# Performance work log

Hardware: AMD Instinct MI355X
Metric: run time of the kernel (lower is better)

## Reference

```python
import jax, jax.numpy as jnp
import numpy as np

D_MODEL = 1024
NUM_HEADS = 16
D_K = D_MODEL // NUM_HEADS


def setup_inputs() -> dict:
    key = jax.random.key(0)
    k1, k2, k3, k4 = jax.random.split(key, 4)
    x = jax.random.normal(k1, (2, 2048, D_MODEL), dtype=jnp.float32)
    # qkv_proj: Linear(d_model, 3*d_model, bias=False); stored as [in, out] for x @ W
    W_qkv = jax.random.normal(k2, (D_MODEL, 3 * D_MODEL), dtype=jnp.float32) * (1.0 / np.sqrt(D_MODEL))
    W_out = jax.random.normal(k3, (D_MODEL, D_MODEL), dtype=jnp.float32) * (1.0 / np.sqrt(D_MODEL))
    b_out = jax.random.normal(k4, (D_MODEL,), dtype=jnp.float32) * 0.01
    return {"x": x, "W_qkv": W_qkv, "W_out": W_out, "b_out": b_out}


def reference(x, W_qkv, W_out, b_out):
    B, N, C = x.shape
    scale = 1.0 / np.sqrt(D_K)
    qkv = (x @ W_qkv).reshape(B, N, 3, NUM_HEADS, D_K)
    qkv = jnp.transpose(qkv, (2, 0, 3, 1, 4))  # [3, B, H, N, d_k]
    q, k, v = qkv[0], qkv[1], qkv[2]
    scores = jnp.einsum("bhqd,bhkd->bhqk", q, k) * scale  # [B,H,N,N]
    attn = jax.nn.softmax(scores, axis=-1)
    out = jnp.einsum("bhqk,bhkd->bhqd", attn, v)  # [B,H,N,d_k]
    out = jnp.transpose(out, (0, 2, 1, 3)).reshape(B, N, C)
    return out @ W_out + b_out
```

## Files before the change

kernel.cpp:

```cpp
#include <hip/hip_runtime.h>
#include <cstdint>

typedef __bf16 bf16_t;
typedef __bf16 bf16x8 __attribute__((ext_vector_type(8)));
typedef float  f32x4  __attribute__((ext_vector_type(4)));
typedef uint32_t u32x4 __attribute__((ext_vector_type(4)));

#define MFMA16(a,b,c) __builtin_amdgcn_mfma_f32_16x16x32_bf16((a),(b),(c),0,0,0)

__device__ __forceinline__ void gload_lds16(const bf16_t* g, bf16_t* l) {
  __builtin_amdgcn_global_load_lds(
      (const __attribute__((address_space(1))) unsigned int*)g,
      (__attribute__((address_space(3))) unsigned int*)l,
      16, 0, 0);
}

__device__ __forceinline__ uint32_t cvt_pk_bf16(float lo, float hi) {
  uint32_t r;
  asm("v_cvt_pk_bf16_f32 %0, %1, %2" : "=v"(r) : "v"(lo), "v"(hi));
  return r;
}

__global__ void k_conv_x(const float* __restrict__ x, bf16_t* __restrict__ xb) {
  int i = blockIdx.x * blockDim.x + threadIdx.x;
  const float4* p = reinterpret_cast<const float4*>(x) + (size_t)i * 2;
  float4 a = p[0], b = p[1];
  bf16x8 v;
  v[0]=(bf16_t)a.x; v[1]=(bf16_t)a.y; v[2]=(bf16_t)a.z; v[3]=(bf16_t)a.w;
  v[4]=(bf16_t)b.x; v[5]=(bf16_t)b.y; v[6]=(bf16_t)b.z; v[7]=(bf16_t)b.w;
  *reinterpret_cast<bf16x8*>(xb + (size_t)i * 8) = v;
}

__global__ void k_transpose_w(const float* __restrict__ W, bf16_t* __restrict__ WT,
                              int K, int N) {
  __shared__ float tile[32][33];
  int n0 = blockIdx.x * 32, k0 = blockIdx.y * 32;
  int c = threadIdx.x & 31, r8 = threadIdx.x >> 5;
#pragma unroll
  for (int rr = 0; rr < 4; rr++) {
    int r = r8 + rr * 8;
    tile[r][c] = W[(size_t)(k0 + r) * N + n0 + c];
  }
  __syncthreads();
#pragma unroll
  for (int rr = 0; rr < 4; rr++) {
    int r = r8 + rr * 8;
    WT[(size_t)(n0 + r) * K + k0 + c] = (bf16_t)tile[c][r];
  }
}

__global__ void k_vtrans(const bf16_t* __restrict__ V, bf16_t* __restrict__ VT) {
  __shared__ bf16_t t[64 * 72];
  int bi = blockIdx.x;
  int head = bi >> 5, kt = bi & 31;
  int tid = threadIdx.x;
  const bf16_t* src = V + (size_t)head * 131072 + (size_t)kt * 64 * 64;
#pragma unroll
  for (int j = 0; j < 2; j++) {
    int q = tid + 256 * j;
    int key = q >> 3, part = q & 7;
    bf16x8 v = *reinterpret_cast<const bf16x8*>(src + key * 64 + part * 8);
    *reinterpret_cast<bf16x8*>(&t[key * 72 + part * 8]) = v;
  }
  __syncthreads();
  bf16_t* dst = VT + (size_t)head * 131072 + kt * 64;
#pragma unroll
  for (int j = 0; j < 2; j++) {
    int q = tid + 256 * j;
    int dv = q >> 3, part = q & 7;
    bf16x8 v;
#pragma unroll
    for (int e = 0; e < 8; e++) v[e] = t[(part * 8 + e) * 72 + dv];
    *reinterpret_cast<bf16x8*>(dst + (size_t)dv * 2048 + part * 8) = v;
  }
}

template<int EPI>
__global__ __launch_bounds__(256, 2) void k_gemm(
    const bf16_t* __restrict__ A, const bf16_t* __restrict__ BT, int Klen,
    bf16_t* __restrict__ Qo, bf16_t* __restrict__ Ko, bf16_t* __restrict__ Vo,
    const float* __restrict__ bias, float* __restrict__ Out, int Nout) {
  __shared__ bf16_t As[2][4096];
  __shared__ bf16_t Bs[2][4096];
  int tid = threadIdx.x, lane = tid & 63, wid = tid >> 6;
  int row0 = blockIdx.x * 128, col0 = blockIdx.y * 128;
  int wr = wid >> 1, wc = wid & 1;
  int g = lane >> 4, li = lane & 15;

  f32x4 acc[4][4] = {};

  auto stage = [&](int buf, int kt) {
    int k0 = kt * 32;
#pragma unroll
    for (int j = 0; j < 2; j++) {
      int q = tid + 256 * j;
      int r = q >> 2, part = q & 3;
      gload_lds16(A + (size_t)(row0 + r) * Klen + k0 + part * 8,
                  &As[buf][(wid * 64 + j * 256) * 8]);
    }
#pragma unroll
    for (int j = 0; j < 2; j++) {
      int q = tid + 256 * j;
      int r = q >> 2, part = q & 3;
      gload_lds16(BT + (size_t)(col0 + r) * Klen + k0 + part * 8,
                  &Bs[buf][(wid * 64 + j * 256) * 8]);
    }
  };

  int nk = Klen >> 5;
  stage(0, 0);
  for (int kt = 0; kt < nk; kt++) {
    __syncthreads();
    if (kt + 1 < nk) stage((kt + 1) & 1, kt + 1);
    int buf = kt & 1;
    int kl = g * 8;
    bf16x8 a[4], b[4];
#pragma unroll
    for (int m = 0; m < 4; m++)
      a[m] = *reinterpret_cast<const bf16x8*>(&As[buf][(wr * 64 + m * 16 + li) * 32 + kl]);
#pragma unroll
    for (int n = 0; n < 4; n++)
      b[n] = *reinterpret_cast<const bf16x8*>(&Bs[buf][(wc * 64 + n * 16 + li) * 32 + kl]);
#pragma unroll
    for (int m = 0; m < 4; m++)
#pragma unroll
      for (int n = 0; n < 4; n++)
        acc[m][n] = MFMA16(a[m], b[n], acc[m][n]);
  }

#pragma unroll
  for (int m = 0; m < 4; m++) {
    int rg = row0 + wr * 64 + m * 16 + g * 4;
#pragma unroll
    for (int n = 0; n < 4; n++) {
      int cg = col0 + wc * 64 + n * 16 + li;
#pragma unroll
      for (int i = 0; i < 4; i++) {
        float v = acc[m][n][i];
        int row = rg + i;
        if constexpr (EPI == 0) {
          int t = cg >> 10, h = (cg >> 6) & 15, dk = cg & 63;
          int b2 = row >> 11, nn = row & 2047;
          size_t idx = ((size_t)((b2 << 4) + h) * 2048 + nn) * 64 + dk;
          if (t == 0)      Qo[idx] = (bf16_t)(v * 0.18033688011112042f);
          else if (t == 1) Ko[idx] = (bf16_t)v;
          else             Vo[idx] = (bf16_t)v;
        } else {
          Out[(size_t)row * Nout + cg] = v + bias[cg];
        }
      }
    }
  }
}

__global__ __launch_bounds__(256, 4) void k_flash(
    const bf16_t* __restrict__ Q, const bf16_t* __restrict__ K,
    const bf16_t* __restrict__ VT, bf16_t* __restrict__ O) {
  __shared__ bf16_t Ks[2][64 * 64];
  __shared__ bf16_t Vs[2][64 * 64];

  int bi = (blockIdx.x & 7) * 128 + (blockIdx.x >> 3);
  int head = bi >> 5, qt = bi & 31;
  int tid = threadIdx.x, lane = tid & 63, wid = tid >> 6;
  int g = lane >> 4, li = lane & 15;

  const bf16_t* Qh = Q + (size_t)head * 131072 + (size_t)qt * 64 * 64;
  const bf16_t* Kh = K + (size_t)head * 131072;
  const bf16_t* Vh = VT + (size_t)head * 131072;

  bf16x8 qf[2];
  {
    const bf16_t* qrow = Qh + (size_t)(wid * 16 + li) * 64;
    qf[0] = *reinterpret_cast<const bf16x8*>(qrow + g * 8);
    qf[1] = *reinterpret_cast<const bf16x8*>(qrow + 32 + g * 8);
  }

  u32x4 onesw;
  onesw[0] = 0x3F803F80u; onesw[1] = 0x3F803F80u;
  onesw[2] = 0x3F803F80u; onesw[3] = 0x3F803F80u;
  bf16x8 ones = __builtin_bit_cast(bf16x8, onesw);

  f32x4 o[4] = {};
  f32x4 osum = {};
  float mrun = 0.f;

  auto stage = [&](int buf, int t) {
    int kv0 = t * 64;
#pragma unroll
    for (int j = 0; j < 2; j++) {
      int q = tid + 256 * j;
      int key = q >> 3, part = q & 7;
      int sw = (key & 7) ^ (((key >> 3) & 3) << 1);
      gload_lds16(Kh + (size_t)(kv0 + key) * 64 + ((part ^ sw) * 8),
                  &Ks[buf][(wid * 64 + j * 256) * 8]);
    }
#pragma unroll
    for (int j = 0; j < 2; j++) {
      int q = tid + 256 * j;
      int dv = q >> 3, part = q & 7;
      gload_lds16(Vh + (size_t)dv * 2048 + kv0 + ((part ^ (dv & 7)) * 8),
                  &Vs[buf][(wid * 64 + j * 256) * 8]);
    }
  };

  stage(0, 0);
  for (int t = 0; t < 32; t++) {
    __syncthreads();
    if (t + 1 < 32) stage((t + 1) & 1, t + 1);
    int buf = t & 1;
    char* KsB = (char*)&Ks[buf][0];
    char* VsB = (char*)&Vs[buf][0];

    float nm = -mrun;
    f32x4 s[4];
#pragma unroll
    for (int nf = 0; nf < 4; nf++) { s[nf][0]=nm; s[nf][1]=nm; s[nf][2]=nm; s[nf][3]=nm; }
    __builtin_amdgcn_s_setprio(1);
#pragma unroll
    for (int kd = 0; kd < 2; kd++)
#pragma unroll
      for (int nf = 0; nf < 4; nf++) {
        int key = ((li >> 2) << 3) | ((nf & 1) << 2) | (li & 3) | ((nf >> 1) << 5);
        int sw = (key & 7) ^ (((key >> 3) & 3) << 1);
        bf16x8 a = *reinterpret_cast<const bf16x8*>(
            KsB + key * 128 + (((kd * 4 + g) ^ sw) << 4));
        s[nf] = MFMA16(a, qf[kd], s[nf]);
      }
    __builtin_amdgcn_s_setprio(0);

    float t0 = fmaxf(fmaxf(s[0][0], s[0][1]), s[0][2]);
    float t1 = fmaxf(fmaxf(s[0][3], s[1][0]), s[1][1]);
    float t2 = fmaxf(fmaxf(s[1][2], s[1][3]), s[2][0]);
    float t3 = fmaxf(fmaxf(s[2][1], s[2][2]), s[2][3]);
    float t4 = fmaxf(fmaxf(s[3][0], s[3][1]), s[3][2]);
    float pmax = fmaxf(fmaxf(fmaxf(t0, t1), fmaxf(t2, t3)), fmaxf(t4, s[3][3]));

    if (!__all(pmax <= 8.f)) {
      float v = pmax;
      v = fmaxf(v, __shfl_xor(v, 16));
      v = fmaxf(v, __shfl_xor(v, 32));
      float d = fmaxf(v, 0.f);
      float sc = __builtin_amdgcn_exp2f(-d);
      mrun += d;
#pragma unroll
      for (int nf = 0; nf < 4; nf++)
#pragma unroll
        for (int i = 0; i < 4; i++) s[nf][i] -= d;
      float osc[4];
#pragma unroll
      for (int i = 0; i < 4; i++) osc[i] = __shfl(sc, g * 4 + i);
#pragma unroll
      for (int nf = 0; nf < 4; nf++)
#pragma unroll
        for (int i = 0; i < 4; i++) o[nf][i] *= osc[i];
#pragma unroll
      for (int i = 0; i < 4; i++) osum[i] *= osc[i];
    }

#pragma unroll
    for (int nf = 0; nf < 4; nf++)
#pragma unroll
      for (int i = 0; i < 4; i++)
        s[nf][i] = __builtin_amdgcn_exp2f(s[nf][i]);

    u32x4 w0, w1;
    w0[0] = cvt_pk_bf16(s[0][0], s[0][1]);
    w0[1] = cvt_pk_bf16(s[0][2], s[0][3]);
    w0[2] = cvt_pk_bf16(s[1][0], s[1][1]);
    w0[3] = cvt_pk_bf16(s[1][2], s[1][3]);
    w1[0] = cvt_pk_bf16(s[2][0], s[2][1]);
    w1[1] = cvt_pk_bf16(s[2][2], s[2][3]);
    w1[2] = cvt_pk_bf16(s[3][0], s[3][1]);
    w1[3] = cvt_pk_bf16(s[3][2], s[3][3]);
    bf16x8 pa0 = __builtin_bit_cast(bf16x8, w0);
    bf16x8 pa1 = __builtin_bit_cast(bf16x8, w1);

    __builtin_amdgcn_s_setprio(1);
    osum = MFMA16(pa0, ones, osum);
    osum = MFMA16(pa1, ones, osum);
#pragma unroll
    for (int nfv = 0; nfv < 4; nfv++) {
      int dv = nfv * 16 + li;
      bf16x8 b0 = *reinterpret_cast<const bf16x8*>(
          VsB + dv * 128 + ((g * 16) ^ ((dv & 7) << 4)));
      o[nfv] = MFMA16(pa0, b0, o[nfv]);
      bf16x8 b1 = *reinterpret_cast<const bf16x8*>(
          VsB + dv * 128 + ((64 + g * 16) ^ ((dv & 7) << 4)));
      o[nfv] = MFMA16(pa1, b1, o[nfv]);
    }
    __builtin_amdgcn_s_setprio(0);
  }

  int b2 = head >> 4, h = head & 15;
#pragma unroll
  for (int i = 0; i < 4; i++) {
    float inv = 1.f / osum[i];
    int n = qt * 64 + wid * 16 + g * 4 + i;
    size_t base = ((size_t)b2 * 2048 + n) * 1024 + h * 64;
#pragma unroll
    for (int nfv = 0; nfv < 4; nfv++)
      O[base + nfv * 16 + li] = (bf16_t)(o[nfv][i] * inv);
  }
}

extern "C" void kernel_launch(void* const* d_in, const int* in_sizes, int n_in,
                              void* d_out, int out_size, void* d_ws, size_t ws_size,
                              hipStream_t stream) {
  const float* x    = (const float*)d_in[0];
  const float* Wqkv = (const float*)d_in[1];
  const float* Wout = (const float*)d_in[2];
  const float* bout = (const float*)d_in[3];
  float* out = (float*)d_out;

  char* ws = (char*)d_ws;
  bf16_t* xb    = (bf16_t*)(ws);
  bf16_t* wqkvT = (bf16_t*)(ws + ((size_t)8  << 20));
  bf16_t* woutT = (bf16_t*)(ws + ((size_t)14 << 20));
  bf16_t* qw    = (bf16_t*)(ws + ((size_t)16 << 20));
  bf16_t* kw    = (bf16_t*)(ws + ((size_t)24 << 20));
  bf16_t* vw    = (bf16_t*)(ws + ((size_t)32 << 20));
  bf16_t* vtw   = (bf16_t*)(ws + ((size_t)40 << 20));
  bf16_t* ow    = (bf16_t*)(ws + ((size_t)48 << 20));

  k_conv_x<<<2048, 256, 0, stream>>>(x, xb);
  k_transpose_w<<<dim3(96, 32), 256, 0, stream>>>(Wqkv, wqkvT, 1024, 3072);
  k_transpose_w<<<dim3(32, 32), 256, 0, stream>>>(Wout, woutT, 1024, 1024);
  k_gemm<0><<<dim3(32, 24), 256, 0, stream>>>(xb, wqkvT, 1024, qw, kw, vw,
                                              nullptr, nullptr, 0);
  k_vtrans<<<1024, 256, 0, stream>>>(vw, vtw);
  k_flash<<<1024, 256, 0, stream>>>(qw, kw, vtw, ow);
  k_gemm<1><<<dim3(32, 8), 256, 0, stream>>>(ow, woutT, 1024,
                                             nullptr, nullptr, nullptr,
                                             bout, out, 1024);
}
```

Before: 125.2 us.

## Double query rows per flash block and use 64-row tiles for output GEMM

The flash kernel now processes 128 query rows per block, two 16-row groups per wave. Each K and V fragment read from LDS is reused across both groups, which halves K/V staging traffic per query and the block count. The output GEMM is templated to use 64-row tiles, doubling its grid to 512 blocks so more CUs are busy. The trade-offs are higher register pressure in flash (launch bounds relaxed from 4 to 2), fewer flash blocks (512) for latency hiding, and more B-tile reloads in the output GEMM.

```diff
diff --git a/kernel.cpp b/kernel.cpp
--- a/kernel.cpp
+++ b/kernel.cpp
@@ -75,35 +75,37 @@
   }
 }
 
-template<int EPI>
+template<int EPI, int MT>
 __global__ __launch_bounds__(256, 2) void k_gemm(
     const bf16_t* __restrict__ A, const bf16_t* __restrict__ BT, int Klen,
     bf16_t* __restrict__ Qo, bf16_t* __restrict__ Ko, bf16_t* __restrict__ Vo,
     const float* __restrict__ bias, float* __restrict__ Out, int Nout) {
-  __shared__ bf16_t As[2][4096];
+  constexpr int WM = MT / 2;
+  constexpr int MF = WM / 16;
+  __shared__ bf16_t As[2][MT * 32];
   __shared__ bf16_t Bs[2][4096];
   int tid = threadIdx.x, lane = tid & 63, wid = tid >> 6;
-  int row0 = blockIdx.x * 128, col0 = blockIdx.y * 128;
+  int row0 = blockIdx.x * MT, col0 = blockIdx.y * 128;
   int wr = wid >> 1, wc = wid & 1;
   int g = lane >> 4, li = lane & 15;
 
-  f32x4 acc[4][4] = {};
+  f32x4 acc[MF][4] = {};
 
   auto stage = [&](int buf, int kt) {
     int k0 = kt * 32;
 #pragma unroll
-    for (int j = 0; j < 2; j++) {
+    for (int j = 0; j < MT / 64; j++) {
       int q = tid + 256 * j;
       int r = q >> 2, part = q & 3;
       gload_lds16(A + (size_t)(row0 + r) * Klen + k0 + part * 8,
-                  &As[buf][(wid * 64 + j * 256) * 8]);
+                  &As[buf][q * 8]);
     }
 #pragma unroll
     for (int j = 0; j < 2; j++) {
       int q = tid + 256 * j;
       int r = q >> 2, part = q & 3;
       gload_lds16(BT + (size_t)(col0 + r) * Klen + k0 + part * 8,
-                  &Bs[buf][(wid * 64 + j * 256) * 8]);
+                  &Bs[buf][q * 8]);
     }
   };
 
@@ -114,23 +116,23 @@
     if (kt + 1 < nk) stage((kt + 1) & 1, kt + 1);
     int buf = kt & 1;
     int kl = g * 8;
-    bf16x8 a[4], b[4];
-#pragma unroll
-    for (int m = 0; m < 4; m++)
-      a[m] = *reinterpret_cast<const bf16x8*>(&As[buf][(wr * 64 + m * 16 + li) * 32 + kl]);
+    bf16x8 a[MF], b[4];
+#pragma unroll
+    for (int m = 0; m < MF; m++)
+      a[m] = *reinterpret_cast<const bf16x8*>(&As[buf][(wr * WM + m * 16 + li) * 32 + kl]);
 #pragma unroll
     for (int n = 0; n < 4; n++)
       b[n] = *reinterpret_cast<const bf16x8*>(&Bs[buf][(wc * 64 + n * 16 + li) * 32 + kl]);
 #pragma unroll
-    for (int m = 0; m < 4; m++)
+    for (int m = 0; m < MF; m++)
 #pragma unroll
       for (int n = 0; n < 4; n++)
         acc[m][n] = MFMA16(a[m], b[n], acc[m][n]);
   }
 
 #pragma unroll
-  for (int m = 0; m < 4; m++) {
-    int rg = row0 + wr * 64 + m * 16 + g * 4;
+  for (int m = 0; m < MF; m++) {
+    int rg = row0 + wr * WM + m * 16 + g * 4;
 #pragma unroll
     for (int n = 0; n < 4; n++) {
       int cg = col0 + wc * 64 + n * 16 + li;
@@ -153,26 +155,27 @@
   }
 }
 
-__global__ __launch_bounds__(256, 4) void k_flash(
+__global__ __launch_bounds__(256, 2) void k_flash(
     const bf16_t* __restrict__ Q, const bf16_t* __restrict__ K,
     const bf16_t* __restrict__ VT, bf16_t* __restrict__ O) {
   __shared__ bf16_t Ks[2][64 * 64];
   __shared__ bf16_t Vs[2][64 * 64];
 
-  int bi = (blockIdx.x & 7) * 128 + (blockIdx.x >> 3);
-  int head = bi >> 5, qt = bi & 31;
+  int bi = (blockIdx.x & 7) * 64 + (blockIdx.x >> 3);
+  int head = bi >> 4, qt = bi & 15;
   int tid = threadIdx.x, lane = tid & 63, wid = tid >> 6;
   int g = lane >> 4, li = lane & 15;
 
-  const bf16_t* Qh = Q + (size_t)head * 131072 + (size_t)qt * 64 * 64;
+  const bf16_t* Qh = Q + (size_t)head * 131072 + (size_t)qt * 128 * 64;
   const bf16_t* Kh = K + (size_t)head * 131072;
   const bf16_t* Vh = VT + (size_t)head * 131072;
 
-  bf16x8 qf[2];
-  {
-    const bf16_t* qrow = Qh + (size_t)(wid * 16 + li) * 64;
-    qf[0] = *reinterpret_cast<const bf16x8*>(qrow + g * 8);
-    qf[1] = *reinterpret_cast<const bf16x8*>(qrow + 32 + g * 8);
+  bf16x8 qf[2][2];
+#pragma unroll
+  for (int rg = 0; rg < 2; rg++) {
+    const bf16_t* qrow = Qh + (size_t)(wid * 32 + rg * 16 + li) * 64;
+    qf[rg][0] = *reinterpret_cast<const bf16x8*>(qrow + g * 8);
+    qf[rg][1] = *reinterpret_cast<const bf16x8*>(qrow + 32 + g * 8);
   }
 
   u32x4 onesw;
@@ -180,9 +183,9 @@
   onesw[2] = 0x3F803F80u; onesw[3] = 0x3F803F80u;
   bf16x8 ones = __builtin_bit_cast(bf16x8, onesw);
 
-  f32x4 o[4] = {};
-  f32x4 osum = {};
-  float mrun = 0.f;
+  f32x4 o[2][4] = {};
+  f32x4 osum[2] = {};
+  float mrun[2] = {0.f, 0.f};
 
   auto stage = [&](int buf, int t) {
     int kv0 = t * 64;
@@ -192,14 +195,14 @@
       int key = q >> 3, part = q & 7;
       int sw = (key & 7) ^ (((key >> 3) & 3) << 1);
       gload_lds16(Kh + (size_t)(kv0 + key) * 64 + ((part ^ sw) * 8),
-                  &Ks[buf][(wid * 64 + j * 256) * 8]);
+                  &Ks[buf][(tid + j * 256) * 8]);
     }
 #pragma unroll
     for (int j = 0; j < 2; j++) {
       int q = tid + 256 * j;
       int dv = q >> 3, part = q & 7;
       gload_lds16(Vh + (size_t)dv * 2048 + kv0 + ((part ^ (dv & 7)) * 8),
-                  &Vs[buf][(wid * 64 + j * 256) * 8]);
+                  &Vs[buf][(tid + j * 256) * 8]);
     }
   };
 
@@ -211,95 +214,126 @@
     char* KsB = (char*)&Ks[buf][0];
     char* VsB = (char*)&Vs[buf][0];
 
-    float nm = -mrun;
-    f32x4 s[4];
-#pragma unroll
-    for (int nf = 0; nf < 4; nf++) { s[nf][0]=nm; s[nf][1]=nm; s[nf][2]=nm; s[nf][3]=nm; }
-    __builtin_amdgcn_s_setprio(1);
+    bf16x8 ka[2][4];
 #pragma unroll
     for (int kd = 0; kd < 2; kd++)
 #pragma unroll
       for (int nf = 0; nf < 4; nf++) {
         int key = ((li >> 2) << 3) | ((nf & 1) << 2) | (li & 3) | ((nf >> 1) << 5);
         int sw = (key & 7) ^ (((key >> 3) & 3) << 1);
-        bf16x8 a = *reinterpret_cast<const bf16x8*>(
+        ka[kd][nf] = *reinterpret_cast<const bf16x8*>(
             KsB + key * 128 + (((kd * 4 + g) ^ sw) << 4));
-        s[nf] = MFMA16(a, qf[kd], s[nf]);
+      }
+
+    f32x4 s[2][4];
+#pragma unroll
+    for (int rg = 0; rg < 2; rg++) {
+      float nm = -mrun[rg];
+#pragma unroll
+      for (int nf = 0; nf < 4; nf++) {
+        s[rg][nf][0] = nm; s[rg][nf][1] = nm; s[rg][nf][2] = nm; s[rg][nf][3] = nm;
+      }
+    }
+    __builtin_amdgcn_s_setprio(1);
+#pragma unroll
+    for (int kd = 0; kd < 2; kd++)
+#pragma unroll
+      for (int nf = 0; nf < 4; nf++) {
+        s[0][nf] = MFMA16(ka[kd][nf], qf[0][kd], s[0][nf]);
+        s[1][nf] = MFMA16(ka[kd][nf], qf[1][kd], s[1][nf]);
       }
     __builtin_amdgcn_s_setprio(0);
 
-    float t0 = fmaxf(fmaxf(s[0][0], s[0][1]), s[0][2]);
-    float t1 = fmaxf(fmaxf(s[0][3], s[1][0]), s[1][1]);
-    float t2 = fmaxf(fmaxf(s[1][2], s[1][3]), s[2][0]);
-    float t3 = fmaxf(fmaxf(s[2][1], s[2][2]), s[2][3]);
-    float t4 = fmaxf(fmaxf(s[3][0], s[3][1]), s[3][2]);
-    float pmax = fmaxf(fmaxf(fmaxf(t0, t1), fmaxf(t2, t3)), fmaxf(t4, s[3][3]));
-
-    if (!__all(pmax <= 8.f)) {
-      float v = pmax;
-      v = fmaxf(v, __shfl_xor(v, 16));
-      v = fmaxf(v, __shfl_xor(v, 32));
-      float d = fmaxf(v, 0.f);
-      float sc = __builtin_amdgcn_exp2f(-d);
-      mrun += d;
+    float pmax[2];
+#pragma unroll
+    for (int rg = 0; rg < 2; rg++) {
+      float t0 = fmaxf(fmaxf(s[rg][0][0], s[rg][0][1]), s[rg][0][2]);
+      float t1 = fmaxf(fmaxf(s[rg][0][3], s[rg][1][0]), s[rg][1][1]);
+      float t2 = fmaxf(fmaxf(s[rg][1][2], s[rg][1][3]), s[rg][2][0]);
+      float t3 = fmaxf(fmaxf(s[rg][2][1], s[rg][2][2]), s[rg][2][3]);
+      float t4 = fmaxf(fmaxf(s[rg][3][0], s[rg][3][1]), s[rg][3][2]);
+      pmax[rg] = fmaxf(fmaxf(fmaxf(t0, t1), fmaxf(t2, t3)), fmaxf(t4, s[rg][3][3]));
+    }
+
+    bool ok = (pmax[0] <= 8.f) & (pmax[1] <= 8.f);
+    if (!__all(ok)) {
+#pragma unroll
+      for (int rg = 0; rg < 2; rg++) {
+        float v = pmax[rg];
+        v = fmaxf(v, __shfl_xor(v, 16));
+        v = fmaxf(v, __shfl_xor(v, 32));
+        float d = fmaxf(v, 0.f);
+        float sc = __builtin_amdgcn_exp2f(-d);
+        mrun[rg] += d;
+#pragma unroll
+        for (int nf = 0; nf < 4; nf++)
+#pragma unroll
+          for (int i = 0; i < 4; i++) s[rg][nf][i] -= d;
+        float osc[4];
+#pragma unroll
+        for (int i = 0; i < 4; i++) osc[i] = __shfl(sc, g * 4 + i);
+#pragma unroll
+        for (int nf = 0; nf < 4; nf++)
+#pragma unroll
+          for (int i = 0; i < 4; i++) o[rg][nf][i] *= osc[i];
+#pragma unroll
+        for (int i = 0; i < 4; i++) osum[rg][i] *= osc[i];
+      }
+    }
+
+    bf16x8 pa[2][2];
+#pragma unroll
+    for (int rg = 0; rg < 2; rg++) {
 #pragma unroll
       for (int nf = 0; nf < 4; nf++)
 #pragma unroll
-        for (int i = 0; i < 4; i++) s[nf][i] -= d;
-      float osc[4];
-#pragma unroll
-      for (int i = 0; i < 4; i++) osc[i] = __shfl(sc, g * 4 + i);
-#pragma unroll
-      for (int nf = 0; nf < 4; nf++)
-#pragma unroll
-        for (int i = 0; i < 4; i++) o[nf][i] *= osc[i];
-#pragma unroll
-      for (int i = 0; i < 4; i++) osum[i] *= osc[i];
-    }
-
-#pragma unroll
-    for (int nf = 0; nf < 4; nf++)
-#pragma unroll
-      for (int i = 0; i < 4; i++)
-        s[nf][i] = __builtin_amdgcn_exp2f(s[nf][i]);
-
-    u32x4 w0, w1;
-    w0[0] = cvt_pk_bf16(s[0][0], s[0][1]);
-    w0[1] = cvt_pk_bf16(s[0][2], s[0][3]);
-    w0[2] = cvt_pk_bf16(s[1][0], s[1][1]);
-    w0[3] = cvt_pk_bf16(s[1][2], s[1][3]);
-    w1[0] = cvt_pk_bf16(s[2][0], s[2][1]);
-    w1[1] = cvt_pk_bf16(s[2][2], s[2][3]);
-    w1[2] = cvt_pk_bf16(s[3][0], s[3][1]);
-    w1[3] = cvt_pk_bf16(s[3][2], s[3][3]);
-    bf16x8 pa0 = __builtin_bit_cast(bf16x8, w0);
-    bf16x8 pa1 = __builtin_bit_cast(bf16x8, w1);
+        for (int i = 0; i < 4; i++)
+          s[rg][nf][i] = __builtin_amdgcn_exp2f(s[rg][nf][i]);
+      u32x4 w0, w1;
+      w0[0] = cvt_pk_bf16(s[rg][0][0], s[rg][0][1]);
+      w0[1] = cvt_pk_bf16(s[rg][0][2], s[rg][0][3]);
+      w0[2] = cvt_pk_bf16(s[rg][1][0], s[rg][1][1]);
+      w0[3] = cvt_pk_bf16(s[rg][1][2], s[rg][1][3]);
+      w1[0] = cvt_pk_bf16(s[rg][2][0], s[rg][2][1]);
+      w1[1] = cvt_pk_bf16(s[rg][2][2], s[rg][2][3]);
+      w1[2] = cvt_pk_bf16(s[rg][3][0], s[rg][3][1]);
+      w1[3] = cvt_pk_bf16(s[rg][3][2], s[rg][3][3]);
+      pa[rg][0] = __builtin_bit_cast(bf16x8, w0);
+      pa[rg][1] = __builtin_bit_cast(bf16x8, w1);
+    }
 
     __builtin_amdgcn_s_setprio(1);
-    osum = MFMA16(pa0, ones, osum);
-    osum = MFMA16(pa1, ones, osum);
+    osum[0] = MFMA16(pa[0][0], ones, osum[0]);
+    osum[0] = MFMA16(pa[0][1], ones, osum[0]);
+    osum[1] = MFMA16(pa[1][0], ones, osum[1]);
+    osum[1] = MFMA16(pa[1][1], ones, osum[1]);
 #pragma unroll
     for (int nfv = 0; nfv < 4; nfv++) {
       int dv = nfv * 16 + li;
       bf16x8 b0 = *reinterpret_cast<const bf16x8*>(
           VsB + dv * 128 + ((g * 16) ^ ((dv & 7) << 4)));
-      o[nfv] = MFMA16(pa0, b0, o[nfv]);
       bf16x8 b1 = *reinterpret_cast<const bf16x8*>(
           VsB + dv * 128 + ((64 + g * 16) ^ ((dv & 7) << 4)));
-      o[nfv] = MFMA16(pa1, b1, o[nfv]);
+      o[0][nfv] = MFMA16(pa[0][0], b0, o[0][nfv]);
+      o[0][nfv] = MFMA16(pa[0][1], b1, o[0][nfv]);
+      o[1][nfv] = MFMA16(pa[1][0], b0, o[1][nfv]);
+      o[1][nfv] = MFMA16(pa[1][1], b1, o[1][nfv]);
     }
     __builtin_amdgcn_s_setprio(0);
   }
 
   int b2 = head >> 4, h = head & 15;
 #pragma unroll
-  for (int i = 0; i < 4; i++) {
-    float inv = 1.f / osum[i];
-    int n = qt * 64 + wid * 16 + g * 4 + i;
-    size_t base = ((size_t)b2 * 2048 + n) * 1024 + h * 64;
-#pragma unroll
-    for (int nfv = 0; nfv < 4; nfv++)
-      O[base + nfv * 16 + li] = (bf16_t)(o[nfv][i] * inv);
+  for (int rg = 0; rg < 2; rg++) {
+#pragma unroll
+    for (int i = 0; i < 4; i++) {
+      float inv = 1.f / osum[rg][i];
+      int n = qt * 128 + wid * 32 + rg * 16 + g * 4 + i;
+      size_t base = ((size_t)b2 * 2048 + n) * 1024 + h * 64;
+#pragma unroll
+      for (int nfv = 0; nfv < 4; nfv++)
+        O[base + nfv * 16 + li] = (bf16_t)(o[rg][nfv][i] * inv);
+    }
   }
 }
 
@@ -325,11 +359,11 @@
   k_conv_x<<<2048, 256, 0, stream>>>(x, xb);
   k_transpose_w<<<dim3(96, 32), 256, 0, stream>>>(Wqkv, wqkvT, 1024, 3072);
   k_transpose_w<<<dim3(32, 32), 256, 0, stream>>>(Wout, woutT, 1024, 1024);
-  k_gemm<0><<<dim3(32, 24), 256, 0, stream>>>(xb, wqkvT, 1024, qw, kw, vw,
-                                              nullptr, nullptr, 0);
+  k_gemm<0,128><<<dim3(32, 24), 256, 0, stream>>>(xb, wqkvT, 1024, qw, kw, vw,
+                                                  nullptr, nullptr, 0);
   k_vtrans<<<1024, 256, 0, stream>>>(vw, vtw);
-  k_flash<<<1024, 256, 0, stream>>>(qw, kw, vtw, ow);
-  k_gemm<1><<<dim3(32, 8), 256, 0, stream>>>(ow, woutT, 1024,
-                                             nullptr, nullptr, nullptr,
-                                             bout, out, 1024);
-}
+  k_flash<<<512, 256, 0, stream>>>(qw, kw, vtw, ow);
+  k_gemm<1,64><<<dim3(64, 8), 256, 0, stream>>>(ow, woutT, 1024,
+                                                nullptr, nullptr, nullptr,
+                                                bout, out, 1024);
+}
```

Measured after the change: 118.9 us. -5.0%, faster.
